# Kernel optimization log

Hardware: AMD Instinct MI355X
Metric: run time of the kernel (lower is better)

## Reference

```python
import jax, jax.numpy as jnp
import numpy as np
import math

B, T, D, H = 2, 2048, 1024, 16
DH = D // H          # 64
NB = DH // 2         # 32 rotary pairs
EPS = 1e-5


def setup_inputs() -> dict:
    key = jax.random.key(0)
    ks = jax.random.split(key, 20)
    x = jax.random.normal(ks[0], (B, T, D), dtype=jnp.float32)
    angles = jax.random.uniform(ks[1], (B, H, T, NB), dtype=jnp.float32) * (2.0 * math.pi)
    cos_a = jnp.cos(angles)
    sin_a = jnp.sin(angles)
    sigma = jax.random.uniform(ks[2], (B, T, H, NB), dtype=jnp.float32)
    causal_mask = jnp.triu(jnp.ones((T, T), dtype=bool), k=1)  # True above diag -> masked
    w = lambda k, i, o: jax.random.normal(k, (i, o), dtype=jnp.float32) * 0.02
    return {
        "x": x, "cos_a": cos_a, "sin_a": sin_a, "sigma": sigma, "causal_mask": causal_mask,
        "ln1_g": jnp.ones((D,), jnp.float32), "ln1_b": jnp.zeros((D,), jnp.float32),
        "wq": w(ks[3], D, D), "bq": jnp.zeros((D,), jnp.float32),
        "wk": w(ks[4], D, D), "bk": jnp.zeros((D,), jnp.float32),
        "wv": w(ks[5], D, D), "bv": jnp.zeros((D,), jnp.float32),
        "wo": w(ks[6], D, D), "bo": jnp.zeros((D,), jnp.float32),
        "ln2_g": jnp.ones((D,), jnp.float32), "ln2_b": jnp.zeros((D,), jnp.float32),
        "w1": w(ks[7], D, 4 * D), "b1": jnp.zeros((4 * D,), jnp.float32),
        "w2": w(ks[8], 4 * D, D), "b2": jnp.zeros((D,), jnp.float32),
    }


def _layer_norm(x, g, b):
    mu = jnp.mean(x, axis=-1, keepdims=True)
    var = jnp.mean(jnp.square(x - mu), axis=-1, keepdims=True)
    return (x - mu) * jax.lax.rsqrt(var + EPS) * g + b


def _apply_rope(q, cos_a, sin_a):
    # q: (B,H,T,DH); rotate even/odd pairs by per-pair angles (B,H,T,NB)
    q1 = q[..., 0::2]
    q2 = q[..., 1::2]
    re = q1 * cos_a - q2 * sin_a
    im = q1 * sin_a + q2 * cos_a
    return jnp.stack([re, im], axis=-1).reshape(q.shape)


def reference(x, cos_a, sin_a, sigma, causal_mask,
              ln1_g, ln1_b, wq, bq, wk, bk, wv, bv, wo, bo,
              ln2_g, ln2_b, w1, b1, w2, b2):
    h = _layer_norm(x, ln1_g, ln1_b)
    Q = (h @ wq + bq).reshape(B, T, H, DH).transpose(0, 2, 1, 3)
    K = (h @ wk + bk).reshape(B, T, H, DH).transpose(0, 2, 1, 3)
    V = (h @ wv + bv).reshape(B, T, H, DH).transpose(0, 2, 1, 3)
    Q = _apply_rope(Q, cos_a, sin_a)
    K = _apply_rope(K, cos_a, sin_a)
    # per-(B,H,T) temperature from mean uncertainty
    temp = 1.0 + jnp.mean(sigma, axis=-1).transpose(0, 2, 1)  # (B,H,T)
    scale = math.sqrt(DH)
    scores = jnp.einsum("bhtd,bhsd->bhts", Q, K) / (scale * temp[..., None])
    scores = jnp.where(causal_mask[None, None], -jnp.inf, scores)
    attn = jax.nn.softmax(scores, axis=-1)
    out = jnp.einsum("bhts,bhsd->bhtd", attn, V)
    out = out.transpose(0, 2, 1, 3).reshape(B, T, D)
    x = x + (out @ wo + bo)
    h2 = _layer_norm(x, ln2_g, ln2_b)
    ffn = jax.nn.gelu(h2 @ w1 + b1, approximate=False) @ w2 + b2
    return x + ffn
```

## Files before the change

kernel.cpp:

```cpp
#include <hip/hip_runtime.h>

typedef unsigned short ushort;
typedef unsigned int uint;

typedef __attribute__((ext_vector_type(8))) short short8;
typedef __attribute__((ext_vector_type(8))) unsigned short ushort8;
typedef __attribute__((ext_vector_type(4))) unsigned short ushort4v;
typedef __attribute__((ext_vector_type(4))) float f32x4;
typedef __attribute__((ext_vector_type(4))) uint uint4v;

#define DEV static __device__ __forceinline__

DEV ushort f2b(float f){
  union { float f; uint u; } v; v.f = f;
  uint u = v.u;
  u += 0x7fffu + ((u >> 16) & 1u);
  return (ushort)(u >> 16);
}
DEV float b2f(ushort h){
  union { uint u; float f; } v; v.u = ((uint)h) << 16;
  return v.f;
}
DEV uint cvt_pk_bf16(float lo, float hi){
  uint r;
  asm("v_cvt_pk_bf16_f32 %0, %1, %2" : "=v"(r) : "v"(lo), "v"(hi));
  return r;
}
DEV ushort f2b1(float f){ return (ushort)cvt_pk_bf16(f, f); }
DEV float exp2v(float x){
  float r;
  asm("v_exp_f32 %0, %1" : "=v"(r) : "v"(x));
  return r;
}
DEV float gelu_f(float x){
  float z = fabsf(x) * 0.70710678118654752f;
  float t = __builtin_amdgcn_rcpf(1.f + 0.3275911f * z);
  float poly = t * (0.254829592f + t * (-0.284496736f + t * (1.421413741f +
               t * (-1.453152027f + t * 1.061405429f))));
  float e = exp2v(-z * z * 1.44269504088896f);
  float erf_abs = 1.f - poly * e;
  float erf_s = copysignf(erf_abs, x);
  return 0.5f * x * (1.f + erf_s);
}

constexpr int Bc = 2, Tc = 2048, Dc = 1024, Hc = 16, DHc = 64, NBc = 32;
constexpr int Rc = Bc * Tc;
constexpr int D4c = 4 * Dc;

__global__ __launch_bounds__(256) void k_transcvt_all(
    const float* __restrict__ wq, const float* __restrict__ wk, const float* __restrict__ wv,
    const float* __restrict__ wo, const float* __restrict__ w1, const float* __restrict__ w2,
    ushort* __restrict__ wqT, ushort* __restrict__ wkT, ushort* __restrict__ wvT,
    ushort* __restrict__ woT, ushort* __restrict__ w1T, ushort* __restrict__ w2T){
  __shared__ float tile[32][33];
  const int bid = blockIdx.x;
  const float* in; ushort* out; int K, N, bx, by;
  if (bid < 4096){
    int seg = bid >> 10, loc = bid & 1023;
    in  = seg == 0 ? wq  : seg == 1 ? wk  : seg == 2 ? wv  : wo;
    out = seg == 0 ? wqT : seg == 1 ? wkT : seg == 2 ? wvT : woT;
    K = 1024; N = 1024; bx = loc & 31; by = loc >> 5;
  } else if (bid < 8192){
    int loc = bid - 4096;
    in = w1; out = w1T; K = 1024; N = 4096; bx = loc & 127; by = loc >> 7;
  } else {
    int loc = bid - 8192;
    in = w2; out = w2T; K = 4096; N = 1024; bx = loc & 31; by = loc >> 5;
  }
  int n0 = bx * 32, k0 = by * 32;
  int c = threadIdx.x & 31, r0 = threadIdx.x >> 5;
#pragma unroll
  for (int i = 0; i < 4; i++){
    int k = r0 + i * 8;
    tile[k][c] = in[(size_t)(k0 + k) * N + n0 + c];
  }
  __syncthreads();
#pragma unroll
  for (int i = 0; i < 4; i++){
    int n = r0 + i * 8;
    out[(size_t)(n0 + n) * K + k0 + c] = f2b(tile[c][n]);
  }
}

__global__ __launch_bounds__(256) void k_ln(const float* __restrict__ x, const float* __restrict__ g,
                                            const float* __restrict__ bb, ushort* __restrict__ out){
  int row = blockIdx.x, tid = threadIdx.x;
  const f32x4* xr = (const f32x4*)(x + (size_t)row * Dc);
  f32x4 v = xr[tid];
  float s  = v.x + v.y + v.z + v.w;
  float ss = v.x*v.x + v.y*v.y + v.z*v.z + v.w*v.w;
#pragma unroll
  for (int off = 32; off > 0; off >>= 1){
    s  += __shfl_xor(s,  off, 64);
    ss += __shfl_xor(ss, off, 64);
  }
  __shared__ float red[2][4];
  int w = tid >> 6;
  if ((tid & 63) == 0){ red[0][w] = s; red[1][w] = ss; }
  __syncthreads();
  s  = red[0][0] + red[0][1] + red[0][2] + red[0][3];
  ss = red[1][0] + red[1][1] + red[1][2] + red[1][3];
  float mu  = s * (1.f / Dc);
  float var = ss * (1.f / Dc) - mu * mu;
  float rs  = rsqrtf(var + 1e-5f);
  f32x4 gv = ((const f32x4*)g)[tid];
  f32x4 bv = ((const f32x4*)bb)[tid];
  ushort4v o;
  o.x = f2b((v.x - mu) * rs * gv.x + bv.x);
  o.y = f2b((v.y - mu) * rs * gv.y + bv.y);
  o.z = f2b((v.z - mu) * rs * gv.z + bv.z);
  o.w = f2b((v.w - mu) * rs * gv.w + bv.w);
  ((ushort4v*)(out + (size_t)row * Dc))[tid] = o;
}

#define GLDS(src, dst) __builtin_amdgcn_global_load_lds( \
    (const __attribute__((address_space(1))) void*)(src), \
    (__attribute__((address_space(3))) void*)(dst), 16, 0, 0)

#define STAGE128(nb_, k0_) do { \
  _Pragma("unroll") \
  for (int i_ = 0; i_ < 4; i_++){ \
    int chunk_ = w * 4 + i_; \
    GLDS(A  + (size_t)(m0 + chunk_ * 8 + rloc) * K + (k0_) + gsrc * 8, &SM[nb_][0][chunk_ * 512]); \
    GLDS(Bt + (size_t)(n0 + chunk_ * 8 + rloc) * K + (k0_) + gsrc * 8, &SM[nb_][1][chunk_ * 512]); \
  } \
} while(0)

#define GEMM_CORE(cb_) do { \
  _Pragma("unroll") \
  for (int ks = 0; ks < 2; ks++){ \
    const int gs = (ks * 4 + lg) ^ l7; \
    short8 aF[4], bF[4]; \
    _Pragma("unroll") \
    for (int mi = 0; mi < 4; mi++) aF[mi] = *(const short8*)&SM[cb_][0][(arow + mi * 16) * 64 + gs * 8]; \
    _Pragma("unroll") \
    for (int ni = 0; ni < 4; ni++) bF[ni] = *(const short8*)&SM[cb_][1][(brow + ni * 16) * 64 + gs * 8]; \
    _Pragma("unroll") \
    for (int mi = 0; mi < 4; mi++) \
      _Pragma("unroll") \
      for (int ni = 0; ni < 4; ni++) \
        acc[mi][ni] = __builtin_amdgcn_mfma_f32_16x16x32_bf16(aF[mi], bF[ni], acc[mi][ni], 0, 0, 0); \
  } \
} while(0)

template<int OUT_BF16, int ACT_GELU, int HAS_RES>
__global__ __launch_bounds__(256) void k_gemm(const ushort* __restrict__ A, const ushort* __restrict__ Bt,
                                              const float* __restrict__ bias, const float* __restrict__ resid,
                                              void* __restrict__ Cout, int M, int N, int K){
  __shared__ ushort SM[2][2][8192];
  const int tid = threadIdx.x;
  const int m0 = blockIdx.y * 128, n0 = blockIdx.x * 128;
  const int w = tid >> 6, lane = tid & 63;
  const int wr = w >> 1, wc = w & 1;
  const int la15 = lane & 15, lg = lane >> 4, l7 = lane & 7;
  const int rloc = lane >> 3, gsrc = (lane & 7) ^ rloc;

  f32x4 acc[4][4];
#pragma unroll
  for (int i = 0; i < 4; i++)
#pragma unroll
    for (int j = 0; j < 4; j++) acc[i][j] = f32x4{0.f, 0.f, 0.f, 0.f};

  const int arow = wr * 64 + la15;
  const int brow = wc * 64 + la15;

  STAGE128(0, 0);
  __syncthreads();
  const int NT = K >> 6;
  for (int t = 0; t < NT; t++){
    const int cb = t & 1;
    if (t + 1 < NT) STAGE128(cb ^ 1, (t + 1) << 6);
    GEMM_CORE(cb);
    __syncthreads();
  }

  if (OUT_BF16){
    ushort* Cs = &SM[0][0][0];
#pragma unroll
    for (int mi = 0; mi < 4; mi++)
#pragma unroll
      for (int ni = 0; ni < 4; ni++){
        int ccl = wc * 64 + ni * 16 + la15;
        float bv = bias[n0 + ccl];
        f32x4 a4 = acc[mi][ni];
#pragma unroll
        for (int r = 0; r < 4; r++){
          int rl = wr * 64 + mi * 16 + lg * 4 + r;
          float v = a4[r] + bv;
          if (ACT_GELU) v = gelu_f(v);
          Cs[rl * 136 + ccl] = f2b1(v);
        }
      }
    __syncthreads();
#pragma unroll
    for (int p = 0; p < 8; p++){
      int row = p * 16 + (tid >> 4);
      int col = (tid & 15) * 8;
      ushort8 vv = *(const ushort8*)&Cs[row * 136 + col];
      *(ushort8*)((ushort*)Cout + (size_t)(m0 + row) * N + n0 + col) = vv;
    }
  } else {
#pragma unroll
    for (int mi = 0; mi < 4; mi++)
#pragma unroll
      for (int ni = 0; ni < 4; ni++){
        int cc = n0 + wc * 64 + ni * 16 + la15;
        float bv = bias[cc];
        f32x4 a4 = acc[mi][ni];
#pragma unroll
        for (int r = 0; r < 4; r++){
          int rr = m0 + wr * 64 + mi * 16 + lg * 4 + r;
          float v = a4[r] + bv;
          if (HAS_RES) v += resid[(size_t)rr * N + cc];
          ((float*)Cout)[(size_t)rr * N + cc] = v;
        }
      }
  }
}

__global__ __launch_bounds__(256) void k_gemm_qkv(const ushort* __restrict__ A, const ushort* __restrict__ Bt,
                                                  const float* __restrict__ bq_, const float* __restrict__ bk_,
                                                  const float* __restrict__ bv_, ushort* __restrict__ oq,
                                                  ushort* __restrict__ ok, ushort* __restrict__ ovt,
                                                  const float* __restrict__ cosa, const float* __restrict__ sina,
                                                  int K){
  __shared__ ushort SM[2][2][8192];
  const int tid = threadIdx.x;
  const int m0 = blockIdx.y * 128, n0 = blockIdx.x * 128;
  const int w = tid >> 6, lane = tid & 63;
  const int wr = w >> 1, wc = w & 1;
  const int la15 = lane & 15, lg = lane >> 4, l7 = lane & 7;
  const int rloc = lane >> 3, gsrc = (lane & 7) ^ rloc;

  f32x4 acc[4][4];
#pragma unroll
  for (int i = 0; i < 4; i++)
#pragma unroll
    for (int j = 0; j < 4; j++) acc[i][j] = f32x4{0.f, 0.f, 0.f, 0.f};

  const int arow = wr * 64 + la15;
  const int brow = wc * 64 + la15;

  STAGE128(0, 0);
  __syncthreads();
  const int NT = K >> 6;
  for (int t = 0; t < NT; t++){
    const int cb = t & 1;
    if (t + 1 < NT) STAGE128(cb ^ 1, (t + 1) << 6);
    GEMM_CORE(cb);
    __syncthreads();
  }
  __syncthreads();

  const int sel = n0 >> 10;
  ushort* Cs = &SM[0][0][0];
  if (sel < 2){
    const float* bias = sel == 0 ? bq_ : bk_;
    ushort* o = sel == 0 ? oq : ok;
#pragma unroll
    for (int mi = 0; mi < 4; mi++)
#pragma unroll
      for (int ni = 0; ni < 4; ni++){
        int ccl = wc * 64 + ni * 16 + la15;
        float bv = bias[(n0 & 1023) + ccl];
        f32x4 a4 = acc[mi][ni];
#pragma unroll
        for (int r = 0; r < 4; r++){
          int rl = wr * 64 + mi * 16 + lg * 4 + r;
          Cs[rl * 136 + ccl] = f2b1(a4[r] + bv);
        }
      }
    __syncthreads();
#pragma unroll
    for (int p = 0; p < 8; p++){
      int row = p * 16 + (tid >> 4);
      int col = (tid & 15) * 8;
      ushort8 vv = *(const ushort8*)&Cs[row * 136 + col];
      int rr = m0 + row;
      int bb2 = rr >> 11, tt2 = rr & 2047;
      int cg = (n0 & 1023) + col;
      int hh2 = cg >> 6;
      int nb0 = (cg & 63) >> 1;
      size_t ai = ((size_t)(bb2 * Hc + hh2) * Tc + tt2) * NBc + nb0;
      f32x4 cv = *(const f32x4*)(cosa + ai);
      f32x4 sv = *(const f32x4*)(sina + ai);
      ushort8 ov;
#pragma unroll
      for (int j2 = 0; j2 < 4; j2++){
        float x1 = b2f((ushort)vv[2 * j2]), x2 = b2f((ushort)vv[2 * j2 + 1]);
        uint pk = cvt_pk_bf16(x1 * cv[j2] - x2 * sv[j2], x1 * sv[j2] + x2 * cv[j2]);
        ov[2 * j2]     = (ushort)(pk & 0xffff);
        ov[2 * j2 + 1] = (ushort)(pk >> 16);
      }
      *(ushort8*)(o + (size_t)rr * Dc + cg) = ov;
    }
  } else {
#pragma unroll
    for (int mi = 0; mi < 4; mi++)
#pragma unroll
      for (int ni = 0; ni < 4; ni++){
        int ccl = wc * 64 + ni * 16 + la15;
        float bv = bv_[(n0 - 2048) + ccl];
        f32x4 a4 = acc[mi][ni];
#pragma unroll
        for (int r = 0; r < 4; r++){
          int rl = wr * 64 + mi * 16 + lg * 4 + r;
          Cs[ccl * 136 + rl] = f2b1(a4[r] + bv);
        }
      }
    __syncthreads();
    const int bb = m0 >> 11, t0 = m0 & 2047;
#pragma unroll
    for (int p = 0; p < 8; p++){
      int nl = p * 16 + (tid >> 4);
      int tl = (tid & 15) * 8;
      ushort8 vv = *(const ushort8*)&Cs[nl * 136 + tl];
      int ng = (n0 - 2048) + nl;
      *(ushort8*)(ovt + ((size_t)(bb * 1024 + ng) << 11) + t0 + tl) = vv;
    }
  }
}

__global__ __launch_bounds__(256) void k_iscale(const float* __restrict__ sigma, float* __restrict__ isc){
  int idx = blockIdx.x * 256 + threadIdx.x;
  int hh = idx & 15;
  int t  = (idx >> 4) & 2047;
  int b  = idx >> 15;
  const f32x4* sp = (const f32x4*)(sigma + (size_t)idx * NBc);
  float s = 0.f;
#pragma unroll
  for (int i = 0; i < 8; i++){ f32x4 v = sp[i]; s += v.x + v.y + v.z + v.w; }
  isc[(b * Hc + hh) * Tc + t] = 1.44269504088896f / (8.f * (1.f + s * (1.f / NBc)));
}

__global__ __launch_bounds__(64) void k_attn_mfma(const ushort* __restrict__ qb, const ushort* __restrict__ kb,
                                                  const ushort* __restrict__ vtb, const float* __restrict__ isc,
                                                  ushort* __restrict__ ao){
  __shared__ ushort smem[8192];
  const int bid = blockIdx.x;
  const int bh = bid & 31, b = bh >> 4, h = bh & 15;
  const int qt = 63 - (bid >> 5);
  const int lane = threadIdx.x;
  const int la15 = lane & 15, lg = lane >> 4, l7 = lane & 7;
  const int q0w = qt * 32;

  short8 qf[2][2];
  float iscv[2];
#pragma unroll
  for (int sub = 0; sub < 2; sub++){
    int qg = q0w + sub * 16 + la15;
    size_t rb = (size_t)(b * Tc + qg) * Dc + h * DHc;
    qf[sub][0] = *(const short8*)(qb + rb + lg * 8);
    qf[sub][1] = *(const short8*)(qb + rb + 32 + lg * 8);
    iscv[sub] = isc[bh * Tc + qg];
  }

  f32x4 O[2][4];
#pragma unroll
  for (int sub = 0; sub < 2; sub++)
#pragma unroll
    for (int dt = 0; dt < 4; dt++) O[sub][dt] = f32x4{0.f, 0.f, 0.f, 0.f};
  float lacc[2] = {0.f, 0.f};

  const ushort* kbase  = kb + (size_t)b * Tc * Dc + h * DHc;
  const ushort* vtbase = vtb + (size_t)bh * DHc * Tc;
  const int ktmax = q0w + 31;

  const int Rl = lane >> 3, sl = lane & 7;
  const int gV = sl ^ (Rl & 7);

#define STAGE_KV(kt_) do { \
  _Pragma("unroll") \
  for (int i_ = 0; i_ < 8; i_++){ \
    int R_ = i_ * 8 + Rl; \
    int gk_ = sl ^ ((R_ & 3) ^ (((R_ >> 3) & 3) << 1)); \
    GLDS(kbase + (size_t)((kt_) + R_) * Dc + gk_ * 8, &smem[i_ * 512]); \
    GLDS(vtbase + (size_t)R_ * Tc + (kt_) + gV * 8, &smem[4096 + i_ * 512]); \
  } \
} while(0)

#define COMPUTE_T(kt_) do { \
  _Pragma("unroll") \
  for (int sub = 0; sub < 2; sub++){ \
    f32x4 s_[4]; \
    __builtin_amdgcn_s_setprio(1); \
    _Pragma("unroll") \
    for (int t_ = 0; t_ < 4; t_++){ \
      s_[t_] = f32x4{0.f, 0.f, 0.f, 0.f}; \
      s_[t_] = __builtin_amdgcn_mfma_f32_16x16x32_bf16(kf[t_][0], qf[sub][0], s_[t_], 0, 0, 0); \
      s_[t_] = __builtin_amdgcn_mfma_f32_16x16x32_bf16(kf[t_][1], qf[sub][1], s_[t_], 0, 0, 0); \
    } \
    __builtin_amdgcn_s_setprio(0); \
    const int qg_ = q0w + sub * 16 + la15; \
    const float sc_ = iscv[sub]; \
    const bool diag_ = ((kt_) + 63 > q0w + sub * 16); \
    uint up_[4][2]; \
    float lp_ = 0.f; \
    _Pragma("unroll") \
    for (int t_ = 0; t_ < 4; t_++){ \
      _Pragma("unroll") \
      for (int pr_ = 0; pr_ < 2; pr_++){ \
        float e0_ = exp2v(s_[t_][2 * pr_] * sc_); \
        float e1_ = exp2v(s_[t_][2 * pr_ + 1] * sc_); \
        if (diag_){ \
          int kp0_ = (kt_) + ((t_ >> 1) << 5) + lg * 8 + ((t_ & 1) << 2) + 2 * pr_; \
          if (kp0_ > qg_)     e0_ = 0.f; \
          if (kp0_ + 1 > qg_) e1_ = 0.f; \
        } \
        lp_ += e0_ + e1_; \
        up_[t_][pr_] = cvt_pk_bf16(e0_, e1_); \
      } \
    } \
    lacc[sub] += lp_; \
    __builtin_amdgcn_s_setprio(1); \
    _Pragma("unroll") \
    for (int kh_ = 0; kh_ < 2; kh_++){ \
      union { uint4v w; short8 s8; } pfr_; \
      pfr_.w[0] = up_[kh_ * 2][0];     pfr_.w[1] = up_[kh_ * 2][1]; \
      pfr_.w[2] = up_[kh_ * 2 + 1][0]; pfr_.w[3] = up_[kh_ * 2 + 1][1]; \
      _Pragma("unroll") \
      for (int dt_ = 0; dt_ < 4; dt_++) \
        O[sub][dt_] = __builtin_amdgcn_mfma_f32_16x16x32_bf16(vtf[dt_][kh_], pfr_.s8, O[sub][dt_], 0, 0, 0); \
    } \
    __builtin_amdgcn_s_setprio(0); \
  } \
} while(0)

  STAGE_KV(0);
  asm volatile("s_waitcnt vmcnt(0)" ::: "memory");
  __builtin_amdgcn_sched_barrier(0);

  for (int kt = 0;; kt += 64){
    short8 kf[4][2], vtf[4][2];
#pragma unroll
    for (int t_ = 0; t_ < 4; t_++){
      int r = ((t_ >> 1) << 5) + ((la15 >> 2) << 3) + ((t_ & 1) << 2) + (la15 & 3);
#pragma unroll
      for (int ds = 0; ds < 2; ds++){
        int g = (ds * 4 + lg) ^ ((la15 & 3) ^ ((la15 >> 2) << 1));
        kf[t_][ds] = *(const short8*)&smem[r * 64 + g * 8];
      }
    }
#pragma unroll
    for (int dt = 0; dt < 4; dt++){
      int d = dt * 16 + la15;
#pragma unroll
      for (int kh = 0; kh < 2; kh++){
        int g = (kh * 4 + lg) ^ (la15 & 7);
        vtf[dt][kh] = *(const short8*)&smem[4096 + d * 64 + g * 8];
      }
    }
    asm volatile("s_waitcnt lgkmcnt(0)" ::: "memory");
    __builtin_amdgcn_sched_barrier(0);
    STAGE_KV(kt + 64);
    COMPUTE_T(kt);
    if (kt + 64 > ktmax) break;
    asm volatile("s_waitcnt vmcnt(0)" ::: "memory");
    __builtin_amdgcn_sched_barrier(0);
  }
  asm volatile("s_waitcnt vmcnt(0)" ::: "memory");
  __builtin_amdgcn_sched_barrier(0);

  char* osb = (char*)smem;
#pragma unroll
  for (int sub = 0; sub < 2; sub++){
    float lt = lacc[sub];
    lt += __shfl_xor(lt, 16, 64);
    lt += __shfl_xor(lt, 32, 64);
    float inv = 1.f / lt;
#pragma unroll
    for (int dt = 0; dt < 4; dt++)
#pragma unroll
      for (int pr = 0; pr < 2; pr++){
        uint u = cvt_pk_bf16(O[sub][dt][2 * pr] * inv, O[sub][dt][2 * pr + 1] * inv);
        *(uint*)(osb + (sub * 16 + la15) * 136 + (dt * 16 + lg * 4 + pr * 2) * 2) = u;
      }
  }
#pragma unroll
  for (int it = 0; it < 4; it++){
    int ql = it * 8 + (lane >> 3);
    ushort8 v = *(const ushort8*)(osb + ql * 136 + l7 * 16);
    *(ushort8*)(ao + (size_t)(b * Tc + q0w + ql) * Dc + h * DHc + l7 * 8) = v;
  }
}

extern "C" void kernel_launch(void* const* d_in, const int* in_sizes, int n_in,
                              void* d_out, int out_size, void* d_ws, size_t ws_size,
                              hipStream_t stream){
  (void)in_sizes; (void)n_in; (void)out_size; (void)ws_size;
  const float* x    = (const float*)d_in[0];
  const float* cosa = (const float*)d_in[1];
  const float* sina = (const float*)d_in[2];
  const float* sigma= (const float*)d_in[3];
  const float* ln1g = (const float*)d_in[5];
  const float* ln1b = (const float*)d_in[6];
  const float* wq   = (const float*)d_in[7];
  const float* bq   = (const float*)d_in[8];
  const float* wk   = (const float*)d_in[9];
  const float* bk   = (const float*)d_in[10];
  const float* wv   = (const float*)d_in[11];
  const float* bv   = (const float*)d_in[12];
  const float* wo   = (const float*)d_in[13];
  const float* bo   = (const float*)d_in[14];
  const float* ln2g = (const float*)d_in[15];
  const float* ln2b = (const float*)d_in[16];
  const float* w1   = (const float*)d_in[17];
  const float* b1   = (const float*)d_in[18];
  const float* w2   = (const float*)d_in[19];
  const float* b2   = (const float*)d_in[20];
  float* out = (float*)d_out;

  char* ws = (char*)d_ws;
  constexpr size_t MB = 1024 * 1024;
  ushort* wqT  = (ushort*)(ws +  0 * MB);
  ushort* wkT  = (ushort*)(ws +  2 * MB);
  ushort* wvT  = (ushort*)(ws +  4 * MB);
  ushort* woT  = (ushort*)(ws +  6 * MB);
  ushort* w1T  = (ushort*)(ws +  8 * MB);
  ushort* w2T  = (ushort*)(ws + 16 * MB);
  ushort* hb   = (ushort*)(ws + 24 * MB);
  ushort* qbuf = (ushort*)(ws + 32 * MB);
  ushort* kbuf = (ushort*)(ws + 40 * MB);
  ushort* vtb  = (ushort*)(ws + 48 * MB);
  ushort* aob  = (ushort*)(ws + 56 * MB);
  float*  x2   = (float*)(ws + 64 * MB);
  float*  iscp = (float*)(ws + 80 * MB);
  ushort* g1b  = qbuf;

  k_transcvt_all<<<12288, 256, 0, stream>>>(wq, wk, wv, wo, w1, w2, wqT, wkT, wvT, woT, w1T, w2T);
  k_ln<<<Rc, 256, 0, stream>>>(x, ln1g, ln1b, hb);
  k_gemm_qkv<<<dim3(3 * Dc / 128, Rc / 128), 256, 0, stream>>>(hb, wqT, bq, bk, bv, qbuf, kbuf, vtb,
                                                               cosa, sina, Dc);
  k_iscale<<<(Bc * Tc * Hc) / 256, 256, 0, stream>>>(sigma, iscp);
  k_attn_mfma<<<dim3(2048), 64, 0, stream>>>(qbuf, kbuf, vtb, iscp, aob);
  k_gemm<0, 0, 1><<<dim3(Dc / 128, Rc / 128), 256, 0, stream>>>(aob, woT, bo, x, x2, Rc, Dc, Dc);
  k_ln<<<Rc, 256, 0, stream>>>(x2, ln2g, ln2b, hb);
  k_gemm<1, 1, 0><<<dim3(D4c / 128, Rc / 128), 256, 0, stream>>>(hb, w1T, b1, nullptr, g1b, Rc, D4c, Dc);
  k_gemm<0, 0, 1><<<dim3(Dc / 128, Rc / 128), 256, 0, stream>>>(g1b, w2T, b2, x2, out, Rc, Dc, D4c);
}
```

Baseline: 231.6 us.

## Add 128x64-tile GEMM for N=1024 projections and XCD-aware block swizzle

Adds a GEMM kernel with 128x64 output tiles, used for the output projection and the second FFN projection. With N=1024 the old 128x128 tiling launched only 256 blocks, which underfills the GPU, and the new tiling doubles that. It also remaps block indices so that consecutive tiles land on the same XCD, improving L2 reuse, and applies this to all GEMMs. The cost is lower per-block arithmetic intensity, since the A tile is reloaded twice as often.

```diff
diff --git a/kernel.cpp b/kernel.cpp
--- a/kernel.cpp
+++ b/kernel.cpp
@@ -117,6 +117,13 @@
     (const __attribute__((address_space(1))) void*)(src), \
     (__attribute__((address_space(3))) void*)(dst), 16, 0, 0)
 
+#define XCD_SWZ(bx_, by_, nbx_, nwg_) do{ \
+  int lid_ = blockIdx.y * (nbx_) + blockIdx.x; \
+  int cpx_ = (nwg_) >> 3; \
+  int swz_ = (lid_ & 7) * cpx_ + (lid_ >> 3); \
+  bx_ = swz_ % (nbx_); by_ = swz_ / (nbx_); \
+}while(0)
+
 #define STAGE128(nb_, k0_) do { \
   _Pragma("unroll") \
   for (int i_ = 0; i_ < 4; i_++){ \
@@ -149,7 +156,9 @@
                                               void* __restrict__ Cout, int M, int N, int K){
   __shared__ ushort SM[2][2][8192];
   const int tid = threadIdx.x;
-  const int m0 = blockIdx.y * 128, n0 = blockIdx.x * 128;
+  int bx, by;
+  XCD_SWZ(bx, by, N >> 7, (M >> 7) * (N >> 7));
+  const int m0 = by * 128, n0 = bx * 128;
   const int w = tid >> 6, lane = tid & 63;
   const int wr = w >> 1, wc = w & 1;
   const int la15 = lane & 15, lg = lane >> 4, l7 = lane & 7;
@@ -218,6 +227,82 @@
   }
 }
 
+__global__ __launch_bounds__(256) void k_gemm_n64(const ushort* __restrict__ A, const ushort* __restrict__ Bt,
+                                                  const float* __restrict__ bias, const float* __restrict__ resid,
+                                                  float* __restrict__ Cout, int M, int N, int K){
+  __shared__ ushort SM[2][12288];
+  const int tid = threadIdx.x;
+  int bx, by;
+  XCD_SWZ(bx, by, N >> 6, (M >> 7) * (N >> 6));
+  const int m0 = by * 128, n0 = bx * 64;
+  const int w = tid >> 6, lane = tid & 63;
+  const int la15 = lane & 15, lg = lane >> 4, l7 = lane & 7;
+  const int rloc = lane >> 3, gsrc = (lane & 7) ^ rloc;
+
+  f32x4 acc[2][4];
+#pragma unroll
+  for (int i = 0; i < 2; i++)
+#pragma unroll
+    for (int j = 0; j < 4; j++) acc[i][j] = f32x4{0.f, 0.f, 0.f, 0.f};
+
+  const int arow = w * 32 + la15;
+
+#define STAGE64(nb_, k0_) do { \
+  _Pragma("unroll") \
+  for (int i_ = 0; i_ < 4; i_++){ \
+    int chunk_ = w * 4 + i_; \
+    GLDS(A + (size_t)(m0 + chunk_ * 8 + rloc) * K + (k0_) + gsrc * 8, &SM[nb_][chunk_ * 512]); \
+  } \
+  _Pragma("unroll") \
+  for (int j_ = 0; j_ < 2; j_++){ \
+    int chunk_ = w * 2 + j_; \
+    GLDS(Bt + (size_t)(n0 + chunk_ * 8 + rloc) * K + (k0_) + gsrc * 8, &SM[nb_][8192 + chunk_ * 512]); \
+  } \
+} while(0)
+
+#define CORE64(cb_) do { \
+  _Pragma("unroll") \
+  for (int ks = 0; ks < 2; ks++){ \
+    const int gs = (ks * 4 + lg) ^ l7; \
+    short8 aF[2], bF[4]; \
+    _Pragma("unroll") \
+    for (int mi = 0; mi < 2; mi++) aF[mi] = *(const short8*)&SM[cb_][(arow + mi * 16) * 64 + gs * 8]; \
+    _Pragma("unroll") \
+    for (int ni = 0; ni < 4; ni++) bF[ni] = *(const short8*)&SM[cb_][8192 + (ni * 16 + la15) * 64 + gs * 8]; \
+    _Pragma("unroll") \
+    for (int mi = 0; mi < 2; mi++) \
+      _Pragma("unroll") \
+      for (int ni = 0; ni < 4; ni++) \
+        acc[mi][ni] = __builtin_amdgcn_mfma_f32_16x16x32_bf16(aF[mi], bF[ni], acc[mi][ni], 0, 0, 0); \
+  } \
+} while(0)
+
+  STAGE64(0, 0);
+  __syncthreads();
+  const int NT = K >> 6;
+  for (int t = 0; t < NT; t++){
+    const int cb = t & 1;
+    if (t + 1 < NT) STAGE64(cb ^ 1, (t + 1) << 6);
+    CORE64(cb);
+    __syncthreads();
+  }
+
+#pragma unroll
+  for (int mi = 0; mi < 2; mi++)
+#pragma unroll
+    for (int ni = 0; ni < 4; ni++){
+      int cc = n0 + ni * 16 + la15;
+      float bv = bias[cc];
+      f32x4 a4 = acc[mi][ni];
+#pragma unroll
+      for (int r = 0; r < 4; r++){
+        int rr = m0 + w * 32 + mi * 16 + lg * 4 + r;
+        float v = a4[r] + bv + resid[(size_t)rr * N + cc];
+        Cout[(size_t)rr * N + cc] = v;
+      }
+    }
+}
+
 __global__ __launch_bounds__(256) void k_gemm_qkv(const ushort* __restrict__ A, const ushort* __restrict__ Bt,
                                                   const float* __restrict__ bq_, const float* __restrict__ bk_,
                                                   const float* __restrict__ bv_, ushort* __restrict__ oq,
@@ -226,7 +311,9 @@
                                                   int K){
   __shared__ ushort SM[2][2][8192];
   const int tid = threadIdx.x;
-  const int m0 = blockIdx.y * 128, n0 = blockIdx.x * 128;
+  int bx, by;
+  XCD_SWZ(bx, by, 24, 24 * 32);
+  const int m0 = by * 128, n0 = bx * 128;
   const int w = tid >> 6, lane = tid & 63;
   const int wr = w >> 1, wc = w & 1;
   const int la15 = lane & 15, lg = lane >> 4, l7 = lane & 7;
@@ -533,8 +620,8 @@
                                                                cosa, sina, Dc);
   k_iscale<<<(Bc * Tc * Hc) / 256, 256, 0, stream>>>(sigma, iscp);
   k_attn_mfma<<<dim3(2048), 64, 0, stream>>>(qbuf, kbuf, vtb, iscp, aob);
-  k_gemm<0, 0, 1><<<dim3(Dc / 128, Rc / 128), 256, 0, stream>>>(aob, woT, bo, x, x2, Rc, Dc, Dc);
+  k_gemm_n64<<<dim3(Dc / 64, Rc / 128), 256, 0, stream>>>(aob, woT, bo, x, x2, Rc, Dc, Dc);
   k_ln<<<Rc, 256, 0, stream>>>(x2, ln2g, ln2b, hb);
   k_gemm<1, 1, 0><<<dim3(D4c / 128, Rc / 128), 256, 0, stream>>>(hb, w1T, b1, nullptr, g1b, Rc, D4c, Dc);
-  k_gemm<0, 0, 1><<<dim3(Dc / 128, Rc / 128), 256, 0, stream>>>(g1b, w2T, b2, x2, out, Rc, Dc, D4c);
-}
+  k_gemm_n64<<<dim3(Dc / 64, Rc / 128), 256, 0, stream>>>(g1b, w2T, b2, x2, out, Rc, Dc, D4c);
+}
```

Measured after the change: 227.8 us. About the same (-1.7%).
